# Performance work log

Measured on AMD Instinct MI355X. Metric: run time of the kernel, lower is better.

## Reference

```python
import jax, jax.numpy as jnp
import numpy as np

D_MODEL = 1024
N_HEADS = 16
HEAD_DIM = 64  # 16*64 = 1024
LATENT = 256   # low-rank KV compression dim
NUM_WHEELS = 4
WHEEL_OUT = 256


def setup_inputs() -> dict:
    key = jax.random.key(0)
    ks = jax.random.split(key, 9)
    S = 2048
    s = lambda fan_in: 1.0 / np.sqrt(fan_in)
    return {
        "sketch_emb": jax.random.normal(ks[0], (S, D_MODEL), dtype=jnp.float32),
        "Wq": jax.random.normal(ks[1], (D_MODEL, N_HEADS * HEAD_DIM), dtype=jnp.float32) * s(D_MODEL),
        "Wdkv": jax.random.normal(ks[2], (D_MODEL, LATENT), dtype=jnp.float32) * s(D_MODEL),
        "Wuk": jax.random.normal(ks[3], (LATENT, N_HEADS * HEAD_DIM), dtype=jnp.float32) * s(LATENT),
        "Wuv": jax.random.normal(ks[4], (LATENT, N_HEADS * HEAD_DIM), dtype=jnp.float32) * s(LATENT),
        "Wo": jax.random.normal(ks[5], (N_HEADS * HEAD_DIM, D_MODEL), dtype=jnp.float32) * s(N_HEADS * HEAD_DIM),
        "wheel_W": jax.random.normal(ks[6], (NUM_WHEELS, D_MODEL, WHEEL_OUT), dtype=jnp.float32) * s(D_MODEL),
        "wheel_b": jax.random.normal(ks[7], (NUM_WHEELS, WHEEL_OUT), dtype=jnp.float32) * 0.01,
    }


def reference(sketch_emb, Wq, Wdkv, Wuk, Wuv, Wo, wheel_W, wheel_b):
    S = sketch_emb.shape[0]
    # Multi-head latent attention: per-head Q, shared low-rank KV latent.
    q = (sketch_emb @ Wq).reshape(S, N_HEADS, HEAD_DIM)          # [S,H,D]
    c_kv = sketch_emb @ Wdkv                                      # [S,L]
    k = (c_kv @ Wuk).reshape(S, N_HEADS, HEAD_DIM)                # [S,H,D]
    v = (c_kv @ Wuv).reshape(S, N_HEADS, HEAD_DIM)                # [S,H,D]
    scale = 1.0 / np.sqrt(HEAD_DIM).astype(np.float32)
    scores = jnp.einsum("qhd,khd->hqk", q, k) * scale             # [H,S,S]
    attn = jax.nn.softmax(scores, axis=-1)
    ctx = jnp.einsum("hqk,khd->qhd", attn, v).reshape(S, N_HEADS * HEAD_DIM)
    body = ctx @ Wo                                               # [S,1024]
    # Wheel projections batched as one einsum, then laid out as concat order
    # cat([body, w0, w1, w2, w3], dim=1)
    wheels = jnp.einsum("sd,wde->swe", body, wheel_W) + wheel_b   # [S,W,256]
    wheels = wheels.reshape(S, NUM_WHEELS * WHEEL_OUT)
    return jnp.concatenate([body, wheels], axis=1)                # [S,2048]
```

## Files before the change

kernel.cpp:

```cpp
#include <hip/hip_runtime.h>
#include <math.h>

#define S_LEN 2048
#define DMODEL 1024
#define NHEADS 16
#define HDIM 64
#define QPITCH 1280

typedef _Float16 f16x8 __attribute__((ext_vector_type(8)));
typedef _Float16 f16x4 __attribute__((ext_vector_type(4)));
typedef float    f32x4 __attribute__((ext_vector_type(4)));

__device__ __forceinline__ void gld_lds16(void* lds, const void* g) {
    __builtin_amdgcn_global_load_lds(
        (__attribute__((address_space(1))) void*)(g),
        (__attribute__((address_space(3))) void*)(lds), 16, 0, 0);
}

__device__ __forceinline__ void vm_wait0() { __asm__ __volatile__("s_waitcnt vmcnt(0)" ::: "memory"); }
__device__ __forceinline__ void vm_wait4() { __asm__ __volatile__("s_waitcnt vmcnt(4)" ::: "memory"); }
__device__ __forceinline__ void vm_wait6() { __asm__ __volatile__("s_waitcnt vmcnt(6)" ::: "memory"); }
__device__ __forceinline__ void vm_wait8() { __asm__ __volatile__("s_waitcnt vmcnt(8)" ::: "memory"); }
__device__ __forceinline__ void barrier_raw() {
    __asm__ __volatile__("" ::: "memory");
    __builtin_amdgcn_s_barrier();
    __asm__ __volatile__("" ::: "memory");
}

__device__ __forceinline__ void gemm_core(
    _Float16* sA, _Float16* sB,
    const _Float16* __restrict__ A, int lda,
    const _Float16* __restrict__ Bt, int ldb,
    int nkt,
    _Float16* __restrict__ Cb, int ldcb, int bmode,
    _Float16* __restrict__ Cb2, int ldcb2,
    int bx, int by)
{
    const int tid  = threadIdx.x;
    const int lane = tid & 63;
    const int w    = tid >> 6;
    const int quad = lane >> 4;
    const int c0   = lane & 15;
    const int m0 = by * 128;
    const int n0 = bx * 128;

    const int srow = lane >> 3;
    const int sc   = lane & 7;
    const _Float16* a_src[4]; const _Float16* b_src[4];
    int dstoff[4];
#pragma unroll
    for (int t = 0; t < 4; t++) {
        const int row = w * 32 + t * 8 + srow;
        const int c = sc ^ (row & 7);
        a_src[t] = A  + (size_t)(m0 + row) * lda + c * 8;
        b_src[t] = Bt + (size_t)(n0 + row) * ldb + c * 8;
        dstoff[t] = (w * 32 + t * 8) * 64;
    }

    const int mw = (w & 1) * 64;
    const int nw = (w >> 1) * 64;
    int arow[4], brow[4];
#pragma unroll
    for (int i = 0; i < 4; i++) {
        arow[i] = mw + i * 16 + c0;
        brow[i] = nw + i * 16 + c0;
    }

    f32x4 acc[4][4];
#pragma unroll
    for (int i = 0; i < 4; i++)
#pragma unroll
        for (int j = 0; j < 4; j++) acc[i][j] = (f32x4){0.f, 0.f, 0.f, 0.f};

    auto stage = [&](int buf) {
#pragma unroll
        for (int t = 0; t < 4; t++) {
            gld_lds16(&sA[buf * 8192 + dstoff[t]], a_src[t]); a_src[t] += 64;
            gld_lds16(&sB[buf * 8192 + dstoff[t]], b_src[t]); b_src[t] += 64;
        }
    };
    auto step = [&](int buf) {
#pragma unroll
        for (int ks = 0; ks < 2; ks++) {
            const int cb = ks * 4 + quad;
            f16x8 af[4], bfv[4];
#pragma unroll
            for (int i = 0; i < 4; i++)
                af[i] = *(const f16x8*)&sA[buf * 8192 + arow[i] * 64 + ((cb ^ (arow[i] & 7)) << 3)];
#pragma unroll
            for (int j = 0; j < 4; j++)
                bfv[j] = *(const f16x8*)&sB[buf * 8192 + brow[j] * 64 + ((cb ^ (brow[j] & 7)) << 3)];
#pragma unroll
            for (int i = 0; i < 4; i++)
#pragma unroll
                for (int j = 0; j < 4; j++)
                    acc[i][j] = __builtin_amdgcn_mfma_f32_16x16x32_f16(af[i], bfv[j], acc[i][j], 0, 0, 0);
        }
    };

    stage(0); stage(1);
    int cur = 0;
    for (int kt = 0; kt < nkt; ++kt) {
        if (kt < nkt - 1) vm_wait8(); else vm_wait0();
        barrier_raw();
        if (kt + 2 < nkt) { int nx = cur + 2; if (nx >= 3) nx -= 3; stage(nx); }
        step(cur);
        if (++cur == 3) cur = 0;
    }

#pragma unroll
    for (int i = 0; i < 4; i++) {
#pragma unroll
        for (int reg = 0; reg < 4; reg++) {
            const int m = m0 + mw + i * 16 + quad * 4 + reg;
#pragma unroll
            for (int j = 0; j < 4; j++) {
                const int n = n0 + nw + j * 16 + c0;
                _Float16 hv = (_Float16)acc[i][j][reg];
                if (bmode == 0) {
                    Cb[(size_t)m * ldcb + n] = hv;
                } else {
                    if (n < 1024) Cb[(size_t)m * ldcb + n] = hv;
                    else          Cb2[(size_t)(n - 1024) * ldcb2 + m] = hv;
                }
            }
        }
    }
}

__global__ __launch_bounds__(256) void gemm_qcwf(
    const _Float16* __restrict__ WcT, const _Float16* __restrict__ Wo_f16,
    _Float16* __restrict__ BtWheels,
    const _Float16* __restrict__ emb_f16, const _Float16* __restrict__ Wqc_t,
    _Float16* __restrict__ qc_f16)
{
    __shared__ _Float16 sA[3][8192];
    __shared__ _Float16 sB[3][8192];
    int b = blockIdx.x;
    if (b < 64) {
        gemm_core(&sA[0][0], &sB[0][0], WcT, 1024, Wo_f16, 1024, 16,
                  BtWheels, 1024, 0, nullptr, 0, b >> 3, b & 7);
    } else {
        b -= 64;
        gemm_core(&sA[0][0], &sB[0][0], emb_f16, 1024, Wqc_t, 1024, 16,
                  qc_f16, 1280, 0, nullptr, 0, b >> 4, b & 15);
    }
}

__global__ __launch_bounds__(256) void gemm_kv(
    const _Float16* __restrict__ qc_f16, const _Float16* __restrict__ Wukv_t,
    _Float16* __restrict__ k_f16, _Float16* __restrict__ vT_f16)
{
    __shared__ _Float16 sA[3][8192];
    __shared__ _Float16 sB[3][8192];
    const int b = blockIdx.x;
    gemm_core(&sA[0][0], &sB[0][0], qc_f16 + 1024, 1280, Wukv_t, 256, 4,
              k_f16, 1024, 4, vT_f16, 2048, b >> 4, b & 15);
}

__global__ __launch_bounds__(256) void gemm_fin64(
    const _Float16* __restrict__ A,
    const _Float16* __restrict__ Bt,
    float* __restrict__ out,
    const float* __restrict__ bias)
{
    __shared__ _Float16 sA[3][64 * 64];
    __shared__ _Float16 sB[3][128 * 64];

    const int tid  = threadIdx.x;
    const int lane = tid & 63;
    const int w    = tid >> 6;
    const int quad = lane >> 4;
    const int c0   = lane & 15;

    const int flat = blockIdx.x;
    const int xcd  = flat & 7;
    const int wi   = flat >> 3;
    const int by   = (xcd & 3) * 8 + (wi & 7);
    const int bx   = (xcd >> 2) * 8 + (wi >> 3);
    const int m0 = by * 64;
    const int n0 = bx * 128;

    const int srow = lane >> 3;
    const int sc   = lane & 7;
    const _Float16* a_src[2]; int a_dst[2];
#pragma unroll
    for (int t = 0; t < 2; t++) {
        const int row = t * 32 + w * 8 + srow;
        const int c = sc ^ (row & 7);
        a_src[t] = A + (size_t)(m0 + row) * 1024 + c * 8;
        a_dst[t] = (t * 32 + w * 8) * 64;
    }
    const _Float16* b_src[4]; int b_dst[4];
#pragma unroll
    for (int t = 0; t < 4; t++) {
        const int row = t * 32 + w * 8 + srow;
        const int c = sc ^ (row & 7);
        b_src[t] = Bt + (size_t)(n0 + row) * 1024 + c * 8;
        b_dst[t] = (t * 32 + w * 8) * 64;
    }

    const int mw = (w & 1) * 32;
    const int nw = (w >> 1) * 64;
    int arow[2], brow[4];
#pragma unroll
    for (int i = 0; i < 2; i++) arow[i] = mw + i * 16 + c0;
#pragma unroll
    for (int j = 0; j < 4; j++) brow[j] = nw + j * 16 + c0;

    f32x4 acc[2][4];
#pragma unroll
    for (int i = 0; i < 2; i++)
#pragma unroll
        for (int j = 0; j < 4; j++) acc[i][j] = (f32x4){0.f, 0.f, 0.f, 0.f};

    auto stage = [&](int buf) {
#pragma unroll
        for (int t = 0; t < 2; t++) { gld_lds16(&sA[buf][a_dst[t]], a_src[t]); a_src[t] += 64; }
#pragma unroll
        for (int t = 0; t < 4; t++) { gld_lds16(&sB[buf][b_dst[t]], b_src[t]); b_src[t] += 64; }
    };
    auto step = [&](int buf) {
#pragma unroll
        for (int ks = 0; ks < 2; ks++) {
            const int cb = ks * 4 + quad;
            f16x8 af[2], bfv[4];
#pragma unroll
            for (int i = 0; i < 2; i++)
                af[i] = *(const f16x8*)&sA[buf][arow[i] * 64 + ((cb ^ (arow[i] & 7)) << 3)];
#pragma unroll
            for (int j = 0; j < 4; j++)
                bfv[j] = *(const f16x8*)&sB[buf][brow[j] * 64 + ((cb ^ (brow[j] & 7)) << 3)];
#pragma unroll
            for (int i = 0; i < 2; i++)
#pragma unroll
                for (int j = 0; j < 4; j++)
                    acc[i][j] = __builtin_amdgcn_mfma_f32_16x16x32_f16(af[i], bfv[j], acc[i][j], 0, 0, 0);
        }
    };

    stage(0); stage(1);
    int cur = 0;
    for (int kt = 0; kt < 16; ++kt) {
        if (kt < 15) vm_wait6(); else vm_wait0();
        barrier_raw();
        if (kt + 2 < 16) { int nx = cur + 2; if (nx >= 3) nx -= 3; stage(nx); }
        step(cur);
        if (++cur == 3) cur = 0;
    }

    float bias_v[4];
#pragma unroll
    for (int j = 0; j < 4; j++) bias_v[j] = bias[n0 + nw + j * 16 + c0];
#pragma unroll
    for (int i = 0; i < 2; i++) {
#pragma unroll
        for (int reg = 0; reg < 4; reg++) {
            const int m = m0 + mw + i * 16 + quad * 4 + reg;
#pragma unroll
            for (int j = 0; j < 4; j++) {
                const int n = n0 + nw + j * 16 + c0;
                out[(size_t)m * 2048 + n] = acc[i][j][reg] + bias_v[j];
            }
        }
    }
}

#define SOFT_M2 8.65617024533378f
#define OTP 68

__global__ __launch_bounds__(256) void attn_mfma_kernel(
    const _Float16* __restrict__ qs,
    const _Float16* __restrict__ kk,
    const _Float16* __restrict__ vT,
    float* __restrict__ Opart,
    float* __restrict__ lpart)
{
    __shared__ _Float16 Ks[3][64 * 64];
    __shared__ _Float16 Vt[4][64 * 64];
    __shared__ float    Ot[4][16 * OTP];

    const int flat = blockIdx.x;
    const int g  = flat & 31;
    const int qb = flat >> 5;
    const int h  = g & 15;
    const int kz = g >> 4;
    const int tid  = threadIdx.x;
    const int lane = tid & 63;
    const int w    = tid >> 6;
    const int quad = lane >> 4;
    const int c0   = lane & 15;

    f16x8 qfrag[2][2];
#pragma unroll
    for (int m = 0; m < 2; m++) {
        const _Float16* qrow = qs + (size_t)(qb * 128 + w * 32 + m * 16 + c0) * QPITCH + h * HDIM;
        qfrag[m][0] = *(const f16x8*)(qrow + quad * 8);
        qfrag[m][1] = *(const f16x8*)(qrow + 32 + quad * 8);
    }

    const int srow = lane >> 3;
    const int sc   = lane & 7;
    const _Float16* k_src[2]; const _Float16* v_src[2];
    int dstoff[2];
#pragma unroll
    for (int t = 0; t < 2; t++) {
        const int row = w * 16 + t * 8 + srow;
        const int c = sc ^ (row & 7);
        k_src[t] = kk + (size_t)(kz * 1024 + row) * DMODEL + h * HDIM + c * 8;
        v_src[t] = vT + (size_t)(h * HDIM + row) * S_LEN + kz * 1024 + c * 8;
        dstoff[t] = (w * 16 + t * 8) * 64;
    }

    f32x4 OfragT[2][4];
#pragma unroll
    for (int m = 0; m < 2; m++)
#pragma unroll
        for (int db = 0; db < 4; db++) OfragT[m][db] = (f32x4){0.f, 0.f, 0.f, 0.f};
    f32x4 lacc[2];
    lacc[0] = (f32x4){0.f, 0.f, 0.f, 0.f};
    lacc[1] = (f32x4){0.f, 0.f, 0.f, 0.f};
    f16x4 ones;
    ones[0] = (_Float16)1.f; ones[1] = (_Float16)1.f;
    ones[2] = (_Float16)1.f; ones[3] = (_Float16)1.f;

    f16x4 pf[2][4];

    auto stage = [&](int t) {
        const int kb = t % 3, vb = t & 3;
#pragma unroll
        for (int i = 0; i < 2; i++) {
            gld_lds16(&Ks[kb][dstoff[i]], k_src[i]); k_src[i] += (size_t)64 * DMODEL;
            gld_lds16(&Vt[vb][dstoff[i]], v_src[i]); v_src[i] += 64;
        }
    };

    auto qk = [&](int t, f32x4 (*sf)[4]) {
        const int buf = t % 3;
#pragma unroll
        for (int m = 0; m < 2; m++)
#pragma unroll
            for (int nb = 0; nb < 4; nb++) sf[m][nb] = (f32x4){0.f, 0.f, 0.f, 0.f};
        __builtin_amdgcn_s_setprio(1);
#pragma unroll
        for (int nb = 0; nb < 4; nb++) {
            const int krow = nb * 16 + c0;
#pragma unroll
            for (int ks = 0; ks < 2; ks++) {
                const int cb = ks * 4 + quad;
                f16x8 kfr = *(const f16x8*)&Ks[buf][krow * 64 + ((cb ^ (c0 & 7)) << 3)];
#pragma unroll
                for (int m = 0; m < 2; m++)
                    sf[m][nb] = __builtin_amdgcn_mfma_f32_16x16x32_f16(kfr, qfrag[m][ks], sf[m][nb], 0, 0, 0);
            }
        }
        __builtin_amdgcn_s_setprio(0);
    };

    auto sm = [&](f32x4 (*sf)[4]) {
#pragma unroll
        for (int m = 0; m < 2; m++)
#pragma unroll
            for (int kb = 0; kb < 4; kb++) {
                float p0 = __builtin_amdgcn_exp2f(sf[m][kb][0] - SOFT_M2);
                float p1 = __builtin_amdgcn_exp2f(sf[m][kb][1] - SOFT_M2);
                float p2 = __builtin_amdgcn_exp2f(sf[m][kb][2] - SOFT_M2);
                float p3 = __builtin_amdgcn_exp2f(sf[m][kb][3] - SOFT_M2);
                f16x4 pv;
                pv[0] = (_Float16)p0; pv[1] = (_Float16)p1;
                pv[2] = (_Float16)p2; pv[3] = (_Float16)p3;
                pf[m][kb] = pv;
            }
    };

    auto pv = [&](int t) {
        const int buf = t & 3;
        __builtin_amdgcn_s_setprio(1);
#pragma unroll
        for (int kb = 0; kb < 4; kb++) {
#pragma unroll
            for (int m = 0; m < 2; m++)
                lacc[m] = __builtin_amdgcn_mfma_f32_16x16x16f16(ones, pf[m][kb], lacc[m], 0, 0, 0);
            const int cc = (((kb * 2 + (quad >> 1)) ^ (c0 & 7)) << 3) + (quad & 1) * 4;
#pragma unroll
            for (int db = 0; db < 4; db++) {
                f16x4 vf = *(const f16x4*)&Vt[buf][(db * 16 + c0) * 64 + cc];
#pragma unroll
                for (int m = 0; m < 2; m++)
                    OfragT[m][db] = __builtin_amdgcn_mfma_f32_16x16x16f16(vf, pf[m][kb], OfragT[m][db], 0, 0, 0);
            }
        }
        __builtin_amdgcn_s_setprio(0);
    };

    stage(0); stage(1);
    {
        vm_wait4(); barrier_raw();
        stage(2);
        f32x4 sf[2][4];
        qk(0, sf);
        sm(sf);
    }
    for (int t = 1; t < 16; ++t) {
        if (t < 15) vm_wait4(); else vm_wait0();
        barrier_raw();
        if (t + 2 < 16) stage(t + 2);
        f32x4 sf[2][4];
        qk(t, sf);
        pv(t - 1);
        sm(sf);
    }
    pv(15);

#pragma unroll
    for (int m = 0; m < 2; m++)
        if (quad == 0)
            lpart[(size_t)(kz * 16 + h) * 2048 + qb * 128 + w * 32 + m * 16 + c0] = lacc[m][0];

    float* Otw = &Ot[w][0];
#pragma unroll
    for (int m = 0; m < 2; m++) {
#pragma unroll
        for (int db = 0; db < 4; db++)
            *(f32x4*)&Otw[c0 * OTP + db * 16 + quad * 4] = OfragT[m][db];
        __asm__ __volatile__("s_waitcnt lgkmcnt(0)" ::: "memory");
#pragma unroll
        for (int it = 0; it < 4; it++) {
            const int r = it * 4 + quad;
            f32x4 ov = *(const f32x4*)&Otw[r * OTP + c0 * 4];
            const int row = qb * 128 + w * 32 + m * 16 + r;
            *(f32x4*)&Opart[((size_t)kz * 2048 + row) * 1024 + h * 64 + c0 * 4] = ov;
        }
        __asm__ __volatile__("s_waitcnt lgkmcnt(0)" ::: "memory");
    }
}

__global__ __launch_bounds__(256) void attn_combine_kernel(
    const float* __restrict__ Opart, const float* __restrict__ lpart,
    _Float16* __restrict__ ctx)
{
    const int i = blockIdx.x * 256 + threadIdx.x;
    const int row = i >> 8;
    const int c4  = (i & 255) * 4;
    const int h = c4 >> 6;
    const float l = lpart[(size_t)h * 2048 + row] + lpart[(size_t)(16 + h) * 2048 + row];
    const float inv = 1.0f / l;
    float4 o0 = ((const float4*)(Opart + (size_t)row * 1024))[c4 >> 2];
    float4 o1 = ((const float4*)(Opart + (size_t)(2048 + row) * 1024))[c4 >> 2];
    f16x4 v;
    v[0] = (_Float16)((o0.x + o1.x) * inv);
    v[1] = (_Float16)((o0.y + o1.y) * inv);
    v[2] = (_Float16)((o0.z + o1.z) * inv);
    v[3] = (_Float16)((o0.w + o1.w) * inv);
    *(f16x4*)(ctx + (size_t)row * 1024 + c4) = v;
}

__device__ __forceinline__ void xpose_seg(float (*tile)[33],
    const float* __restrict__ src, _Float16* __restrict__ dst,
    int C, int dpitch, float scale, int bx, int by, int nbase0)
{
    const int r0 = by * 32, c0 = bx * 32;
    const int tr = threadIdx.x >> 5, tc = threadIdx.x & 31;
#pragma unroll
    for (int i = 0; i < 4; i++)
        tile[tr + i * 8][tc] = src[(size_t)(r0 + tr + i * 8) * C + c0 + tc];
    __syncthreads();
    const int nr = threadIdx.x & 31;
    const int k0 = (threadIdx.x >> 5) * 4;
    f16x4 hv;
#pragma unroll
    for (int e = 0; e < 4; e++)
        hv[e] = (_Float16)(tile[k0 + e][nr] * scale);
    *(f16x4*)(dst + (size_t)(nbase0 + c0 + nr) * dpitch + (r0 + k0)) = hv;
}

__global__ __launch_bounds__(256) void megaprep_kernel(
    const float* __restrict__ emb, const float* __restrict__ Wq,
    const float* __restrict__ Wdkv, const float* __restrict__ Wuk,
    const float* __restrict__ Wuv, const float* __restrict__ Wo,
    const float* __restrict__ wheelW, const float* __restrict__ wheelB,
    _Float16* __restrict__ Wqc_t, _Float16* __restrict__ Wukv_t,
    _Float16* __restrict__ Bt_full, _Float16* __restrict__ WcT,
    _Float16* __restrict__ Wo_f16, _Float16* __restrict__ emb_f16,
    float* __restrict__ biasbuf)
{
    __shared__ float tile[32][33];
    int b = blockIdx.x;
    const int tid = threadIdx.x;

    if (b < 1024) { xpose_seg(tile, Wq, Wqc_t, 1024, 1024, 0.125f, b & 31, b >> 5, 0); return; }
    b -= 1024;
    if (b < 256)  { xpose_seg(tile, Wdkv, Wqc_t + 1048576, 256, 1024, 1.f, b & 7, b >> 3, 0); return; }
    b -= 256;
    if (b < 256)  { xpose_seg(tile, Wuk, Wukv_t, 1024, 256, 1.4426950408889634f, b & 31, b >> 5, 0); return; }
    b -= 256;
    if (b < 256)  { xpose_seg(tile, Wuv, Wukv_t + 262144, 1024, 256, 1.f, b & 31, b >> 5, 0); return; }
    b -= 256;
    if (b < 1024) { xpose_seg(tile, Wo, Bt_full, 1024, 1024, 1.f, b & 31, b >> 5, 0); return; }
    b -= 1024;
    if (b < 1024) {
        const int z = b >> 8, rem = b & 255;
        xpose_seg(tile, wheelW + (size_t)z * 262144, WcT, 256, 1024, 1.f,
                  rem & 7, rem >> 3, z * 256);
        return;
    }
    b -= 1024;
    if (b < 1024) {
        const int i = b * 256 + tid;
        float4 f = ((const float4*)Wo)[i];
        f16x4 v;
        v[0] = (_Float16)f.x; v[1] = (_Float16)f.y;
        v[2] = (_Float16)f.z; v[3] = (_Float16)f.w;
        ((f16x4*)Wo_f16)[i] = v;
        return;
    }
    b -= 1024;
    if (b < 2048) {
        const int i = b * 256 + tid;
        float4 f = ((const float4*)emb)[i];
        f16x4 v;
        v[0] = (_Float16)f.x; v[1] = (_Float16)f.y;
        v[2] = (_Float16)f.z; v[3] = (_Float16)f.w;
        ((f16x4*)emb_f16)[i] = v;
        return;
    }
    b -= 2048;
    if (b < 8) {
        const int i = b * 256 + tid;
        biasbuf[i] = (i < 1024) ? 0.f : wheelB[i - 1024];
    }
}

extern "C" void kernel_launch(void* const* d_in, const int* in_sizes, int n_in,
                              void* d_out, int out_size, void* d_ws, size_t ws_size,
                              hipStream_t stream) {
    const float* emb    = (const float*)d_in[0];
    const float* Wq     = (const float*)d_in[1];
    const float* Wdkv   = (const float*)d_in[2];
    const float* Wuk    = (const float*)d_in[3];
    const float* Wuv    = (const float*)d_in[4];
    const float* Wo     = (const float*)d_in[5];
    const float* wheelW = (const float*)d_in[6];
    const float* wheelB = (const float*)d_in[7];
    float* out = (float*)d_out;

    _Float16* ws = (_Float16*)d_ws;
    _Float16* Bt_full = ws;
    _Float16* Wqc_t   = ws + 2097152;
    _Float16* Wukv_t  = ws + 3407872;
    float*    biasbuf = (float*)(ws + 3932160);
    _Float16* WcT     = ws + 3936256;
    _Float16* Wo_f16  = ws + 4984832;
    _Float16* ctx     = ws + 3936256;
    _Float16* emb_f16 = ws + 6033408;
    _Float16* qc_f16  = ws + 8130560;
    _Float16* k_f16   = ws + 10752000;
    _Float16* vT_f16  = ws + 12849152;
    float*    Opart   = (float*)(ws + 14946304);
    float*    lpart   = (float*)(ws + 23334912);

    megaprep_kernel<<<6920, 256, 0, stream>>>(
        emb, Wq, Wdkv, Wuk, Wuv, Wo, wheelW, wheelB,
        Wqc_t, Wukv_t, Bt_full, WcT, Wo_f16, emb_f16, biasbuf);

    gemm_qcwf<<<224, 256, 0, stream>>>(WcT, Wo_f16, Bt_full + (size_t)1024 * 1024,
                                       emb_f16, Wqc_t, qc_f16);

    gemm_kv<<<256, 256, 0, stream>>>(qc_f16, Wukv_t, k_f16, vT_f16);

    attn_mfma_kernel<<<512, 256, 0, stream>>>(qc_f16, k_f16, vT_f16, Opart, lpart);

    attn_combine_kernel<<<2048, 256, 0, stream>>>(Opart, lpart, ctx);

    gemm_fin64<<<512, 256, 0, stream>>>(ctx, Bt_full, out, biasbuf);
}
```

Baseline: 166.2 us.

## Fuse split-K attention combine into attention kernel via atomic last-arriver flags

Removes the separate attention combine launch. Each attention block now bumps a per-(query block, head) atomic counter, and whichever of the two key-split partners arrives second normalizes and sums the partial outputs into ctx. The prep kernel's f32-to-f16 conversion blocks are also made to process four float4s per thread, cutting the grid size. Flags are never reset and the code relies on the count's parity instead, so correctness depends on the workspace starting in a consistent state. The last-arriver also adds extra tail work to the attention kernel.

```diff
diff --git a/kernel.cpp b/kernel.cpp
--- a/kernel.cpp
+++ b/kernel.cpp
@@ -274,11 +274,14 @@
     const _Float16* __restrict__ kk,
     const _Float16* __restrict__ vT,
     float* __restrict__ Opart,
-    float* __restrict__ lpart)
+    float* __restrict__ lpart,
+    int*   __restrict__ flags,
+    _Float16* __restrict__ ctx)
 {
     __shared__ _Float16 Ks[3][64 * 64];
     __shared__ _Float16 Vt[4][64 * 64];
     __shared__ float    Ot[4][16 * OTP];
+    __shared__ int      fin_s;
 
     const int flat = blockIdx.x;
     const int g  = flat & 31;
@@ -433,26 +436,33 @@
         }
         __asm__ __volatile__("s_waitcnt lgkmcnt(0)" ::: "memory");
     }
-}
-
-__global__ __launch_bounds__(256) void attn_combine_kernel(
-    const float* __restrict__ Opart, const float* __restrict__ lpart,
-    _Float16* __restrict__ ctx)
-{
-    const int i = blockIdx.x * 256 + threadIdx.x;
-    const int row = i >> 8;
-    const int c4  = (i & 255) * 4;
-    const int h = c4 >> 6;
-    const float l = lpart[(size_t)h * 2048 + row] + lpart[(size_t)(16 + h) * 2048 + row];
-    const float inv = 1.0f / l;
-    float4 o0 = ((const float4*)(Opart + (size_t)row * 1024))[c4 >> 2];
-    float4 o1 = ((const float4*)(Opart + (size_t)(2048 + row) * 1024))[c4 >> 2];
-    f16x4 v;
-    v[0] = (_Float16)((o0.x + o1.x) * inv);
-    v[1] = (_Float16)((o0.y + o1.y) * inv);
-    v[2] = (_Float16)((o0.z + o1.z) * inv);
-    v[3] = (_Float16)((o0.w + o1.w) * inv);
-    *(f16x4*)(ctx + (size_t)row * 1024 + c4) = v;
+
+    vm_wait0();
+    __syncthreads();
+    if (tid == 0) {
+        __threadfence();
+        int old = atomicAdd(&flags[qb * 16 + h], 1);
+        fin_s = (old & 1);
+    }
+    __syncthreads();
+    if (!fin_s) return;
+    __threadfence();
+
+    for (int i = tid; i < 2048; i += 256) {
+        const int row = qb * 128 + (i >> 4);
+        const int c4  = (i & 15) * 4;
+        const float l = lpart[(size_t)h * 2048 + row] +
+                        lpart[(size_t)(16 + h) * 2048 + row];
+        const float inv = 1.0f / l;
+        f32x4 o0 = *(const f32x4*)&Opart[(size_t)row * 1024 + h * 64 + c4];
+        f32x4 o1 = *(const f32x4*)&Opart[(size_t)(2048 + row) * 1024 + h * 64 + c4];
+        f16x4 v;
+        v[0] = (_Float16)((o0[0] + o1[0]) * inv);
+        v[1] = (_Float16)((o0[1] + o1[1]) * inv);
+        v[2] = (_Float16)((o0[2] + o1[2]) * inv);
+        v[3] = (_Float16)((o0[3] + o1[3]) * inv);
+        *(f16x4*)&ctx[(size_t)row * 1024 + h * 64 + c4] = v;
+    }
 }
 
 __device__ __forceinline__ void xpose_seg(float (*tile)[33],
@@ -505,26 +515,32 @@
         return;
     }
     b -= 1024;
-    if (b < 1024) {
-        const int i = b * 256 + tid;
-        float4 f = ((const float4*)Wo)[i];
-        f16x4 v;
-        v[0] = (_Float16)f.x; v[1] = (_Float16)f.y;
-        v[2] = (_Float16)f.z; v[3] = (_Float16)f.w;
-        ((f16x4*)Wo_f16)[i] = v;
+    if (b < 256) {
+#pragma unroll
+        for (int k = 0; k < 4; k++) {
+            const int i = b * 1024 + k * 256 + tid;
+            float4 f = ((const float4*)Wo)[i];
+            f16x4 v;
+            v[0] = (_Float16)f.x; v[1] = (_Float16)f.y;
+            v[2] = (_Float16)f.z; v[3] = (_Float16)f.w;
+            ((f16x4*)Wo_f16)[i] = v;
+        }
         return;
     }
-    b -= 1024;
-    if (b < 2048) {
-        const int i = b * 256 + tid;
-        float4 f = ((const float4*)emb)[i];
-        f16x4 v;
-        v[0] = (_Float16)f.x; v[1] = (_Float16)f.y;
-        v[2] = (_Float16)f.z; v[3] = (_Float16)f.w;
-        ((f16x4*)emb_f16)[i] = v;
+    b -= 256;
+    if (b < 512) {
+#pragma unroll
+        for (int k = 0; k < 4; k++) {
+            const int i = b * 1024 + k * 256 + tid;
+            float4 f = ((const float4*)emb)[i];
+            f16x4 v;
+            v[0] = (_Float16)f.x; v[1] = (_Float16)f.y;
+            v[2] = (_Float16)f.z; v[3] = (_Float16)f.w;
+            ((f16x4*)emb_f16)[i] = v;
+        }
         return;
     }
-    b -= 2048;
+    b -= 512;
     if (b < 8) {
         const int i = b * 256 + tid;
         biasbuf[i] = (i < 1024) ? 0.f : wheelB[i - 1024];
@@ -558,8 +574,9 @@
     _Float16* vT_f16  = ws + 12849152;
     float*    Opart   = (float*)(ws + 14946304);
     float*    lpart   = (float*)(ws + 23334912);
-
-    megaprep_kernel<<<6920, 256, 0, stream>>>(
+    int*      flags   = (int*)(ws + 23465984);
+
+    megaprep_kernel<<<4616, 256, 0, stream>>>(
         emb, Wq, Wdkv, Wuk, Wuv, Wo, wheelW, wheelB,
         Wqc_t, Wukv_t, Bt_full, WcT, Wo_f16, emb_f16, biasbuf);
 
@@ -568,9 +585,8 @@
 
     gemm_kv<<<256, 256, 0, stream>>>(qc_f16, Wukv_t, k_f16, vT_f16);
 
-    attn_mfma_kernel<<<512, 256, 0, stream>>>(qc_f16, k_f16, vT_f16, Opart, lpart);
-
-    attn_combine_kernel<<<2048, 256, 0, stream>>>(Opart, lpart, ctx);
+    attn_mfma_kernel<<<512, 256, 0, stream>>>(qc_f16, k_f16, vT_f16,
+                                              Opart, lpart, flags, ctx);
 
     gemm_fin64<<<512, 256, 0, stream>>>(ctx, Bt_full, out, biasbuf);
 }
```

After: 204.2 us. 22.9% more time.
